# Kernel optimization log

Hardware: AMD Instinct MI355X
Metric: run time of the kernel (lower is better)

Reference implementation:

```python
import jax, jax.numpy as jnp
import numpy as np

B, T, D, E, V = 16, 256, 512, 512, 32000  # batch, seqlen, embed_dim, encoder_embed_dim, vocab


def setup_inputs() -> dict:
    key = jax.random.key(0)
    ks = jax.random.split(key, 13)
    s = 0.05
    return {
        "prev_output_tokens": jax.random.randint(ks[0], (B, T), 0, V),
        "encoder_out": jax.random.normal(ks[1], (B, E), jnp.float32),
        "embed": jax.random.normal(ks[2], (V, D), jnp.float32) * s,
        "W_ih0": jax.random.normal(ks[3], (4 * D, E + D), jnp.float32) * s,
        "W_hh0": jax.random.normal(ks[4], (4 * D, D), jnp.float32) * s,
        "b_ih0": jax.random.normal(ks[5], (4 * D,), jnp.float32) * s,
        "b_hh0": jax.random.normal(ks[6], (4 * D,), jnp.float32) * s,
        "W_ih1": jax.random.normal(ks[7], (4 * D, D), jnp.float32) * s,
        "W_hh1": jax.random.normal(ks[8], (4 * D, D), jnp.float32) * s,
        "b_ih1": jax.random.normal(ks[9], (4 * D,), jnp.float32) * s,
        "b_hh1": jax.random.normal(ks[10], (4 * D,), jnp.float32) * s,
        "W_out": jax.random.normal(ks[11], (V, D), jnp.float32) * s,
        "b_out": jax.random.normal(ks[12], (V,), jnp.float32) * s,
    }


def _lstm_cell(x, h, c, W_ih, W_hh, b_ih, b_hh):
    # torch.nn.LSTMCell gate order: i, f, g, o
    gates = x @ W_ih.T + b_ih + h @ W_hh.T + b_hh
    i, f, g, o = jnp.split(gates, 4, axis=-1)
    c_new = jax.nn.sigmoid(f) * c + jax.nn.sigmoid(i) * jnp.tanh(g)
    h_new = jax.nn.sigmoid(o) * jnp.tanh(c_new)
    return h_new, c_new


def reference(prev_output_tokens, encoder_out, embed, W_ih0, W_hh0, b_ih0, b_hh0,
              W_ih1, W_hh1, b_ih1, b_hh1, W_out, b_out):
    # padding_idx=0 -> row 0 of the embedding table is zero
    embed = embed.at[0].set(0.0)
    x = embed[prev_output_tokens]          # [B, T, D]  (dropout: eval mode -> identity)
    x = jnp.swapaxes(x, 0, 1)              # [T, B, D]
    bsz = x.shape[1]
    h0 = jnp.zeros((bsz, W_hh0.shape[1]), x.dtype)
    c0, h1, c1 = h0, h0, h0

    def step(carry, x_t):
        h0, c0, h1, c1 = carry
        inp = jnp.concatenate([x_t, encoder_out], axis=1)   # [B, D+E]
        h0, c0 = _lstm_cell(inp, h0, c0, W_ih0, W_hh0, b_ih0, b_hh0)
        h1, c1 = _lstm_cell(h0, h1, c1, W_ih1, W_hh1, b_ih1, b_hh1)
        return (h0, c0, h1, c1), h1

    _, outs = jax.lax.scan(step, (h0, c0, h1, c1), x)       # outs: [T, B, D]
    outs = jnp.swapaxes(outs, 0, 1)                          # [B, T, D]
    return outs @ W_out.T + b_out                            # [B, T, V]
```

## Files before the change

### kernel.cpp

```cpp
#include <hip/hip_runtime.h>
#include <hip/hip_bf16.h>
#include <math.h>

#define BB 16
#define TT 256
#define DD 512
#define EE 512
#define VV 32000
#define G4 2048
#define NTILES (16 * 2 * 250)

typedef __attribute__((ext_vector_type(4))) float f32x4;
typedef __attribute__((ext_vector_type(8))) short bf16x8;
typedef __attribute__((ext_vector_type(4))) unsigned u32x4;

union lf_u { u32x4 q; bf16x8 v; };

#define SENTMASK32 0x40004000u

__device__ __forceinline__ unsigned short f2bf(float x) {
    unsigned u = __float_as_uint(x);
    unsigned r = (u + 0x7FFFu + ((u >> 16) & 1u)) >> 16;
    return (unsigned short)r;
}

__device__ __forceinline__ float sigmoidf_(float x) { return 1.0f / (1.0f + expf(-x)); }

__global__ __launch_bounds__(256) void k_gather(const int* __restrict__ tok,
        const float* __restrict__ embed, unsigned short* __restrict__ Xb) {
    int m = blockIdx.x;
    int tk = tok[m];
    const float* src = embed + (size_t)tk * DD;
    int i = threadIdx.x * 2;
    float vx = 0.f, vy = 0.f;
    if (tk != 0) { float2 v = *(const float2*)&src[i]; vx = v.x; vy = v.y; }
    ushort2 o; o.x = f2bf(vx); o.y = f2bf(vy);
    *(ushort2*)&Xb[(size_t)m * DD + i] = o;
}

__global__ __launch_bounds__(256) void k_cvt(const float* __restrict__ in,
        unsigned short* __restrict__ out, int n4) {
    int i = blockIdx.x * 256 + threadIdx.x;
    if (i >= n4) return;
    float4 v = ((const float4*)in)[i];
    ushort4 o; o.x = f2bf(v.x); o.y = f2bf(v.y); o.z = f2bf(v.z); o.w = f2bf(v.w);
    ((ushort4*)out)[i] = o;
}

__global__ __launch_bounds__(256) void k_cvt_wih0x(const float* __restrict__ Wih0,
        unsigned short* __restrict__ out) {
    int i = blockIdx.x * 256 + threadIdx.x;
    int j = i >> 7;
    int k4 = (i & 127) << 2;
    float4 v = *(const float4*)&Wih0[(size_t)j * (EE + DD) + k4];
    ushort4 o; o.x = f2bf(v.x); o.y = f2bf(v.y); o.z = f2bf(v.z); o.w = f2bf(v.w);
    *(ushort4*)&out[(size_t)j * DD + k4] = o;
}

__global__ __launch_bounds__(256) void k_encterm(const float* __restrict__ enc,
        const float* __restrict__ Wih0, const float* __restrict__ bih0,
        const float* __restrict__ bhh0, float* __restrict__ et) {
    int b = blockIdx.x >> 3, jc = blockIdx.x & 7;
    int tid = threadIdx.x, lane = tid & 63, w = tid >> 6;
    __shared__ float es[EE];
    if (tid < EE / 4) *(float4*)&es[tid * 4] = *(const float4*)&enc[b * EE + tid * 4];
    __syncthreads();
    float4 e0 = *(const float4*)&es[lane * 4];
    float4 e1 = *(const float4*)&es[256 + lane * 4];
    for (int o = 0; o < 64; ++o) {
        int j = jc * 256 + w * 64 + o;
        const float4* Wr = (const float4*)&Wih0[(size_t)j * (EE + DD) + DD];
        float4 w0 = Wr[lane], w1 = Wr[64 + lane];
        float s = w0.x*e0.x + w0.y*e0.y + w0.z*e0.z + w0.w*e0.w
                + w1.x*e1.x + w1.y*e1.y + w1.z*e1.z + w1.w*e1.w;
        #pragma unroll
        for (int off = 32; off; off >>= 1) s += __shfl_xor(s, off);
        if (lane == 0) et[b * G4 + j] = s + bih0[j] + bhh0[j];
    }
}

__global__ __launch_bounds__(256) void k_gemm0(
        const unsigned short* __restrict__ A, const unsigned short* __restrict__ Bm,
        float* __restrict__ C, const float* __restrict__ extra,
        int M, int N, int K) {
    __shared__ __align__(16) unsigned short Alds[128 * 32];
    __shared__ __align__(16) unsigned short Blds[128 * 32];
    int tid = threadIdx.x, lane = tid & 63, w = tid >> 6;
    int wr = w >> 1, wc = w & 1;
    int nwgx = gridDim.x;
    int nwg = nwgx * gridDim.y;
    int lin = blockIdx.y * nwgx + blockIdx.x;
    int cpx = nwg >> 3;
    lin = (lin & 7) * cpx + (lin >> 3);
    int m0 = (lin % nwgx) * 128, n0 = (lin / nwgx) * 128;
    f32x4 acc[4][4];
    #pragma unroll
    for (int i = 0; i < 4; i++)
        #pragma unroll
        for (int j = 0; j < 4; j++) acc[i][j] = (f32x4)0.f;

    const char* Abase = (const char*)A;
    const char* Bbase = (const char*)Bm;
    for (int ks = 0; ks < K; ks += 32) {
        #pragma unroll
        for (int c = 0; c < 2; ++c) {
            int f = (tid + c * 256) * 16;
            int row = f >> 6;
            int inb = f & 63;
            const char* gA = Abase + (((size_t)(m0 + row) * K + ks) * 2 + inb);
            __builtin_amdgcn_global_load_lds(
                (const __attribute__((address_space(1))) void*)gA,
                (__attribute__((address_space(3))) void*)((char*)Alds + f), 16, 0, 0);
            const char* gB = Bbase + (((size_t)(n0 + row) * K + ks) * 2 + inb);
            __builtin_amdgcn_global_load_lds(
                (const __attribute__((address_space(1))) void*)gB,
                (__attribute__((address_space(3))) void*)((char*)Blds + f), 16, 0, 0);
        }
        __syncthreads();
        bf16x8 af[4], bfr[4];
        int r = lane & 15, ko = (lane >> 4) * 8;
        #pragma unroll
        for (int mi = 0; mi < 4; ++mi)
            af[mi] = *(const bf16x8*)&Alds[(wr * 64 + mi * 16 + r) * 32 + ko];
        #pragma unroll
        for (int ni = 0; ni < 4; ++ni)
            bfr[ni] = *(const bf16x8*)&Blds[(wc * 64 + ni * 16 + r) * 32 + ko];
        #pragma unroll
        for (int mi = 0; mi < 4; ++mi)
            #pragma unroll
            for (int ni = 0; ni < 4; ++ni)
                acc[mi][ni] = __builtin_amdgcn_mfma_f32_16x16x32_bf16(af[mi], bfr[ni], acc[mi][ni], 0, 0, 0);
        __syncthreads();
    }
    int cr = (lane >> 4) * 4, cc = lane & 15;
    #pragma unroll
    for (int mi = 0; mi < 4; ++mi) {
        #pragma unroll
        for (int ni = 0; ni < 4; ++ni) {
            int col = n0 + wc * 64 + ni * 16 + cc;
            #pragma unroll
            for (int rr = 0; rr < 4; ++rr) {
                int rowg = m0 + wr * 64 + mi * 16 + cr + rr;
                C[(size_t)rowg * N + col] = acc[mi][ni][rr] + extra[(rowg >> 8) * G4 + col];
            }
        }
    }
}

__device__ __forceinline__ void load16sc(const void* base, lf_u* o) {
    asm volatile(
        "global_load_dwordx4 %0, %16, off sc0 sc1\n\t"
        "global_load_dwordx4 %1, %16, off offset:64 sc0 sc1\n\t"
        "global_load_dwordx4 %2, %16, off offset:128 sc0 sc1\n\t"
        "global_load_dwordx4 %3, %16, off offset:192 sc0 sc1\n\t"
        "global_load_dwordx4 %4, %16, off offset:256 sc0 sc1\n\t"
        "global_load_dwordx4 %5, %16, off offset:320 sc0 sc1\n\t"
        "global_load_dwordx4 %6, %16, off offset:384 sc0 sc1\n\t"
        "global_load_dwordx4 %7, %16, off offset:448 sc0 sc1\n\t"
        "global_load_dwordx4 %8, %16, off offset:512 sc0 sc1\n\t"
        "global_load_dwordx4 %9, %16, off offset:576 sc0 sc1\n\t"
        "global_load_dwordx4 %10, %16, off offset:640 sc0 sc1\n\t"
        "global_load_dwordx4 %11, %16, off offset:704 sc0 sc1\n\t"
        "global_load_dwordx4 %12, %16, off offset:768 sc0 sc1\n\t"
        "global_load_dwordx4 %13, %16, off offset:832 sc0 sc1\n\t"
        "global_load_dwordx4 %14, %16, off offset:896 sc0 sc1\n\t"
        "global_load_dwordx4 %15, %16, off offset:960 sc0 sc1\n\t"
        "s_waitcnt vmcnt(0)"
        : "=&v"(o[0].q), "=&v"(o[1].q), "=&v"(o[2].q), "=&v"(o[3].q),
          "=&v"(o[4].q), "=&v"(o[5].q), "=&v"(o[6].q), "=&v"(o[7].q),
          "=&v"(o[8].q), "=&v"(o[9].q), "=&v"(o[10].q), "=&v"(o[11].q),
          "=&v"(o[12].q), "=&v"(o[13].q), "=&v"(o[14].q), "=&v"(o[15].q)
        : "v"(base)
        : "memory");
}

__device__ __forceinline__ void poll16sc(const void* base, lf_u* o) {
    for (;;) {
        load16sc(base, o);
        unsigned bad = 0;
        #pragma unroll
        for (int kt = 0; kt < 16; ++kt)
            bad |= (o[kt].q.x | o[kt].q.y | o[kt].q.z | o[kt].q.w);
        if (!__any((bad & SENTMASK32) != 0)) return;
    }
}

__device__ __forceinline__ void store8sc(void* addr, unsigned long long v) {
    asm volatile("global_store_dwordx2 %0, %1, off sc0 sc1"
                 :: "v"(addr), "v"(v) : "memory");
}

__global__ __launch_bounds__(256) void k_mega(
        const float* __restrict__ Gx,
        const float* __restrict__ Whh0,
        const float* __restrict__ Wih1, const float* __restrict__ Whh1,
        const float* __restrict__ bih1, const float* __restrict__ bhh1,
        unsigned short* h0hist, unsigned short* outsb,
        const unsigned short* zbuf,
        const unsigned short* __restrict__ Woutb, const float* __restrict__ bout,
        float* __restrict__ out,
        int* ep1, int* tick) {
    __shared__ __align__(16) unsigned char smem[4 * 32 * 512 * 2 + 512];
    __shared__ int idSh;
    const int bid = blockIdx.x;

    if (bid < 64) {
        unsigned short* wfrag = (unsigned short*)smem;
        unsigned short* houts = (unsigned short*)(smem + 4 * 32 * 512 * 2);
        const int l = threadIdx.x;
        const int role = bid >> 5;
        const int blk = bid & 31;
        const int d0 = blk * 16;
        const int r16 = l & 15;
        const int q = (l >> 4) & 3;
        const int ksub = q * 8;
        const int b0 = q * 4;
        const int srow = (l >> 2) & 15;
        const int sseg = l & 3;

        const int nkt = role ? 32 : 16;
        if (l < 64) {
            for (int tile = 0; tile < 4; ++tile) {
                int j = tile * 512 + d0 + r16;
                for (int kt = 0; kt < nkt; ++kt) {
                    const float* src;
                    if (role == 0)    src = Whh0 + (size_t)j * DD + kt * 32 + ksub;
                    else if (kt < 16) src = Wih1 + (size_t)j * DD + kt * 32 + ksub;
                    else              src = Whh1 + (size_t)j * DD + (kt - 16) * 32 + ksub;
                    float4 x = *(const float4*)src;
                    float4 y = *(const float4*)(src + 4);
                    bf16x8 w;
                    w[0] = f2bf(x.x); w[1] = f2bf(x.y); w[2] = f2bf(x.z); w[3] = f2bf(x.w);
                    w[4] = f2bf(y.x); w[5] = f2bf(y.y); w[6] = f2bf(y.z); w[7] = f2bf(y.w);
                    *(bf16x8*)&wfrag[((tile * 32 + kt) * 64 + l) * 8] = w;
                }
            }
        }
        __syncthreads();
        if (l >= 64) return;

        float cst[4] = {0.f, 0.f, 0.f, 0.f};
        lf_u xf[16];

        if (role == 0) {
            for (int t = 0; t < TT; ++t) {
                float gx[4][4];
                #pragma unroll
                for (int ni = 0; ni < 4; ++ni)
                    #pragma unroll
                    for (int rr = 0; rr < 4; ++rr)
                        gx[ni][rr] = Gx[((size_t)(b0 + rr) * TT + t) * G4 + ni * 512 + d0 + r16];

                const char* xb = (const char*)(h0hist + (size_t)t * (BB * DD) + r16 * DD) + q * 16;
                poll16sc(xb, xf);

                f32x4 acc[4];
                #pragma unroll
                for (int ni = 0; ni < 4; ++ni) acc[ni] = (f32x4)0.f;
                #pragma unroll
                for (int kt = 0; kt < 16; ++kt) {
                    #pragma unroll
                    for (int ni = 0; ni < 4; ++ni) {
                        bf16x8 wf = *(const bf16x8*)&wfrag[((ni * 32 + kt) * 64 + l) * 8];
                        acc[ni] = __builtin_amdgcn_mfma_f32_16x16x32_bf16(xf[kt].v, wf, acc[ni], 0, 0, 0);
                    }
                }
                #pragma unroll
                for (int rr = 0; rr < 4; ++rr) {
                    float gi = acc[0][rr] + gx[0][rr], gf = acc[1][rr] + gx[1][rr];
                    float gg = acc[2][rr] + gx[2][rr], go = acc[3][rr] + gx[3][rr];
                    float cn = sigmoidf_(gf) * cst[rr] + sigmoidf_(gi) * tanhf(gg);
                    float hn = sigmoidf_(go) * tanhf(cn);
                    cst[rr] = cn;
                    houts[(b0 + rr) * 16 + r16] = f2bf(hn);
                }
                asm volatile("" ::: "memory");
                {
                    const unsigned short* hp = &houts[srow * 16 + sseg * 4];
                    unsigned long long w8 =  (unsigned long long)hp[0]
                                          | ((unsigned long long)hp[1] << 16)
                                          | ((unsigned long long)hp[2] << 32)
                                          | ((unsigned long long)hp[3] << 48);
                    store8sc(h0hist + (size_t)(t + 1) * (BB * DD) + srow * DD + d0 + sseg * 4, w8);
                }
            }
        } else {
            lf_u hf[16];
            float bin[4];
            #pragma unroll
            for (int ni = 0; ni < 4; ++ni)
                bin[ni] = bih1[ni * 512 + d0 + r16] + bhh1[ni * 512 + d0 + r16];
            for (int t = 0; t < TT; ++t) {
                const char* xb = (const char*)(h0hist + (size_t)(t + 1) * (BB * DD) + r16 * DD) + q * 16;
                poll16sc(xb, xf);

                f32x4 acc[4];
                #pragma unroll
                for (int ni = 0; ni < 4; ++ni)
                    acc[ni] = (f32x4){bin[ni], bin[ni], bin[ni], bin[ni]};
                #pragma unroll
                for (int kt = 0; kt < 16; ++kt) {
                    #pragma unroll
                    for (int ni = 0; ni < 4; ++ni) {
                        bf16x8 wf = *(const bf16x8*)&wfrag[((ni * 32 + kt) * 64 + l) * 8];
                        acc[ni] = __builtin_amdgcn_mfma_f32_16x16x32_bf16(xf[kt].v, wf, acc[ni], 0, 0, 0);
                    }
                }
                const char* hb = (t == 0)
                    ? (const char*)(zbuf + r16 * DD) + q * 16
                    : (const char*)(outsb + ((size_t)r16 * TT + (t - 1)) * DD) + q * 16;
                poll16sc(hb, hf);
                #pragma unroll
                for (int kt = 0; kt < 16; ++kt) {
                    #pragma unroll
                    for (int ni = 0; ni < 4; ++ni) {
                        bf16x8 wf = *(const bf16x8*)&wfrag[((ni * 32 + 16 + kt) * 64 + l) * 8];
                        acc[ni] = __builtin_amdgcn_mfma_f32_16x16x32_bf16(hf[kt].v, wf, acc[ni], 0, 0, 0);
                    }
                }
                #pragma unroll
                for (int rr = 0; rr < 4; ++rr) {
                    float gi = acc[0][rr], gf = acc[1][rr], gg = acc[2][rr], go = acc[3][rr];
                    float cn = sigmoidf_(gf) * cst[rr] + sigmoidf_(gi) * tanhf(gg);
                    float hn = sigmoidf_(go) * tanhf(cn);
                    cst[rr] = cn;
                    houts[(b0 + rr) * 16 + r16] = f2bf(hn);
                }
                asm volatile("" ::: "memory");
                {
                    const unsigned short* hp = &houts[srow * 16 + sseg * 4];
                    unsigned long long w8 =  (unsigned long long)hp[0]
                                          | ((unsigned long long)hp[1] << 16)
                                          | ((unsigned long long)hp[2] << 32)
                                          | ((unsigned long long)hp[3] << 48);
                    store8sc(outsb + ((size_t)srow * TT + t) * DD + d0 + sseg * 4, w8);
                }
                asm volatile("s_waitcnt vmcnt(0)" ::: "memory");
                if (l == 0) {
                    int tv = t + 1;
                    asm volatile("global_store_dword %0, %1, off sc0 sc1"
                                 :: "v"(ep1 + blk * 16), "v"(tv) : "memory");
                }
            }
        }
    } else {
        unsigned short* Alds = (unsigned short*)smem;
        unsigned short* Blds = (unsigned short*)(smem + 8192);
        const int tid = threadIdx.x, lane = tid & 63, w = tid >> 6;
        const int wr = w >> 1, wc = w & 1;

        for (;;) {
            if (tid == 0) idSh = atomicAdd(tick, 1);
            __syncthreads();
            int id = idSh;
            if (id >= NTILES) break;

            int chunk = id / 500;
            int rem   = id % 500;
            int bg    = rem / 250;
            int nt    = rem % 250;
            int t0 = chunk * 16;
            int n0 = nt * 128;
            int target = t0 + 16;

            for (;;) {
                int v;
                asm volatile("global_load_dword %0, %1, off sc0 sc1\n\ts_waitcnt vmcnt(0)"
                             : "=v"(v) : "v"(ep1 + (lane & 31) * 16) : "memory");
                if (__all(v >= target)) break;
                __builtin_amdgcn_s_sleep(4);
            }

            f32x4 acc[4][4];
            #pragma unroll
            for (int i = 0; i < 4; i++)
                #pragma unroll
                for (int j = 0; j < 4; j++) acc[i][j] = (f32x4)0.f;

            for (int ks = 0; ks < DD; ks += 32) {
                #pragma unroll
                for (int c = 0; c < 2; ++c) {
                    int f = (tid + c * 256) * 16;
                    int row = f >> 6;
                    int inb = f & 63;
                    int bb = bg * 8 + (row >> 4);
                    int tt = t0 + (row & 15);
                    const char* gA = (const char*)outsb +
                        (((size_t)bb * TT + tt) * DD + ks) * 2 + inb;
                    __builtin_amdgcn_global_load_lds(
                        (const __attribute__((address_space(1))) void*)gA,
                        (__attribute__((address_space(3))) void*)((char*)Alds + f), 16, 0, 0);
                    const char* gB = (const char*)Woutb +
                        (((size_t)(n0 + row)) * DD + ks) * 2 + inb;
                    __builtin_amdgcn_global_load_lds(
                        (const __attribute__((address_space(1))) void*)gB,
                        (__attribute__((address_space(3))) void*)((char*)Blds + f), 16, 0, 0);
                }
                __syncthreads();
                bf16x8 af[4], bfr[4];
                int r = lane & 15, ko = (lane >> 4) * 8;
                #pragma unroll
                for (int mi = 0; mi < 4; ++mi)
                    af[mi] = *(const bf16x8*)&Alds[(wr * 64 + mi * 16 + r) * 32 + ko];
                #pragma unroll
                for (int ni = 0; ni < 4; ++ni)
                    bfr[ni] = *(const bf16x8*)&Blds[(wc * 64 + ni * 16 + r) * 32 + ko];
                #pragma unroll
                for (int mi = 0; mi < 4; ++mi)
                    #pragma unroll
                    for (int ni = 0; ni < 4; ++ni)
                        acc[mi][ni] = __builtin_amdgcn_mfma_f32_16x16x32_bf16(af[mi], bfr[ni], acc[mi][ni], 0, 0, 0);
                __syncthreads();
            }
            int cr = (lane >> 4) * 4, cc = lane & 15;
            #pragma unroll
            for (int mi = 0; mi < 4; ++mi) {
                #pragma unroll
                for (int ni = 0; ni < 4; ++ni) {
                    int col = n0 + wc * 64 + ni * 16 + cc;
                    #pragma unroll
                    for (int rr = 0; rr < 4; ++rr) {
                        int rloc = wr * 64 + mi * 16 + cr + rr;
                        int bb = bg * 8 + (rloc >> 4);
                        int tt = t0 + (rloc & 15);
                        out[((size_t)bb * TT + tt) * VV + col] = acc[mi][ni][rr] + bout[col];
                    }
                }
            }
        }
    }
}

extern "C" void kernel_launch(void* const* d_in, const int* in_sizes, int n_in,
                              void* d_out, int out_size, void* d_ws, size_t ws_size,
                              hipStream_t stream) {
    const int*   tok   = (const int*)  d_in[0];
    const float* enc   = (const float*)d_in[1];
    const float* embed = (const float*)d_in[2];
    const float* Wih0  = (const float*)d_in[3];
    const float* Whh0  = (const float*)d_in[4];
    const float* bih0  = (const float*)d_in[5];
    const float* bhh0  = (const float*)d_in[6];
    const float* Wih1  = (const float*)d_in[7];
    const float* Whh1  = (const float*)d_in[8];
    const float* bih1  = (const float*)d_in[9];
    const float* bhh1  = (const float*)d_in[10];
    const float* Wout  = (const float*)d_in[11];
    const float* bout  = (const float*)d_in[12];
    float* out = (float*)d_out;

    char* ws = (char*)d_ws;
    size_t off = 0;
    auto alloc = [&](size_t bytes) -> char* {
        char* p = ws + off; off += (bytes + 255) & ~(size_t)255; return p;
    };
    unsigned short* Xb     = (unsigned short*)alloc((size_t)BB * TT * DD * 2);
    unsigned short* Wih0xb = (unsigned short*)alloc((size_t)G4 * DD * 2);
    unsigned short* Woutb  = (unsigned short*)alloc((size_t)VV * DD * 2);
    float*          et     = (float*)alloc((size_t)BB * G4 * sizeof(float));
    float*          Gx     = (float*)alloc((size_t)BB * TT * G4 * sizeof(float));
    unsigned short* outsb  = (unsigned short*)alloc((size_t)BB * TT * DD * 2);
    unsigned short* h0hist = (unsigned short*)alloc((size_t)(TT + 1) * BB * DD * 2);
    unsigned short* zbuf   = (unsigned short*)alloc((size_t)BB * DD * 2);
    int*            ep1    = (int*)alloc(32 * 16 * sizeof(int));
    int*            tick   = (int*)alloc(64 * sizeof(int));

    hipMemsetAsync(h0hist, 0, (size_t)BB * DD * 2, stream);
    hipMemsetAsync(h0hist + (size_t)BB * DD, 0xFF, (size_t)TT * BB * DD * 2, stream);
    hipMemsetAsync(outsb, 0xFF, (size_t)BB * TT * DD * 2, stream);
    hipMemsetAsync(zbuf, 0, (size_t)BB * DD * 2, stream);
    hipMemsetAsync(ep1, 0, 32 * 16 * sizeof(int), stream);
    hipMemsetAsync(tick, 0, 64 * sizeof(int), stream);

    k_gather<<<BB * TT, 256, 0, stream>>>(tok, embed, Xb);
    k_cvt<<<(VV * DD / 4 + 255) / 256, 256, 0, stream>>>(Wout, Woutb, VV * DD / 4);
    k_cvt_wih0x<<<(G4 * DD / 4) / 256, 256, 0, stream>>>(Wih0, Wih0xb);
    k_encterm<<<BB * 8, 256, 0, stream>>>(enc, Wih0, bih0, bhh0, et);

    dim3 g1(BB * TT / 128, G4 / 128);
    k_gemm0<<<g1, 256, 0, stream>>>(Xb, Wih0xb, Gx, et, BB * TT, G4, DD);

    k_mega<<<256, 256, 0, stream>>>(Gx, Whh0, Wih1, Whh1, bih1, bhh1,
                                    h0hist, outsb, zbuf,
                                    Woutb, bout, out, ep1, tick);
}
```

Measured before the change: 1.592 ms.

## Fuse prep kernels and overlap W_out conversion and epoch signaling with recurrence

```diff
diff --git a/kernel.cpp b/kernel.cpp
--- a/kernel.cpp
+++ b/kernel.cpp
@@ -8,6 +8,7 @@
 #define EE 512
 #define VV 32000
 #define G4 2048
+#define NWORK 192
 #define NTILES (16 * 2 * 250)
 
 typedef __attribute__((ext_vector_type(4))) float f32x4;
@@ -17,6 +18,7 @@
 union lf_u { u32x4 q; bf16x8 v; };
 
 #define SENTMASK32 0x40004000u
+#define SENTMASK64 0x4000400040004000ULL
 
 __device__ __forceinline__ unsigned short f2bf(float x) {
     unsigned u = __float_as_uint(x);
@@ -26,56 +28,48 @@
 
 __device__ __forceinline__ float sigmoidf_(float x) { return 1.0f / (1.0f + expf(-x)); }
 
-__global__ __launch_bounds__(256) void k_gather(const int* __restrict__ tok,
-        const float* __restrict__ embed, unsigned short* __restrict__ Xb) {
-    int m = blockIdx.x;
-    int tk = tok[m];
-    const float* src = embed + (size_t)tk * DD;
-    int i = threadIdx.x * 2;
-    float vx = 0.f, vy = 0.f;
-    if (tk != 0) { float2 v = *(const float2*)&src[i]; vx = v.x; vy = v.y; }
-    ushort2 o; o.x = f2bf(vx); o.y = f2bf(vy);
-    *(ushort2*)&Xb[(size_t)m * DD + i] = o;
-}
-
-__global__ __launch_bounds__(256) void k_cvt(const float* __restrict__ in,
-        unsigned short* __restrict__ out, int n4) {
-    int i = blockIdx.x * 256 + threadIdx.x;
-    if (i >= n4) return;
-    float4 v = ((const float4*)in)[i];
-    ushort4 o; o.x = f2bf(v.x); o.y = f2bf(v.y); o.z = f2bf(v.z); o.w = f2bf(v.w);
-    ((ushort4*)out)[i] = o;
-}
-
-__global__ __launch_bounds__(256) void k_cvt_wih0x(const float* __restrict__ Wih0,
-        unsigned short* __restrict__ out) {
-    int i = blockIdx.x * 256 + threadIdx.x;
-    int j = i >> 7;
-    int k4 = (i & 127) << 2;
-    float4 v = *(const float4*)&Wih0[(size_t)j * (EE + DD) + k4];
-    ushort4 o; o.x = f2bf(v.x); o.y = f2bf(v.y); o.z = f2bf(v.z); o.w = f2bf(v.w);
-    *(ushort4*)&out[(size_t)j * DD + k4] = o;
-}
-
-__global__ __launch_bounds__(256) void k_encterm(const float* __restrict__ enc,
-        const float* __restrict__ Wih0, const float* __restrict__ bih0,
+__global__ __launch_bounds__(256) void k_prep(
+        const int* __restrict__ tok, const float* __restrict__ embed,
+        unsigned short* __restrict__ Xb,
+        const float* __restrict__ Wih0, unsigned short* __restrict__ Wih0xb,
+        const float* __restrict__ enc, const float* __restrict__ bih0,
         const float* __restrict__ bhh0, float* __restrict__ et) {
-    int b = blockIdx.x >> 3, jc = blockIdx.x & 7;
-    int tid = threadIdx.x, lane = tid & 63, w = tid >> 6;
     __shared__ float es[EE];
-    if (tid < EE / 4) *(float4*)&es[tid * 4] = *(const float4*)&enc[b * EE + tid * 4];
-    __syncthreads();
-    float4 e0 = *(const float4*)&es[lane * 4];
-    float4 e1 = *(const float4*)&es[256 + lane * 4];
-    for (int o = 0; o < 64; ++o) {
-        int j = jc * 256 + w * 64 + o;
-        const float4* Wr = (const float4*)&Wih0[(size_t)j * (EE + DD) + DD];
-        float4 w0 = Wr[lane], w1 = Wr[64 + lane];
-        float s = w0.x*e0.x + w0.y*e0.y + w0.z*e0.z + w0.w*e0.w
-                + w1.x*e1.x + w1.y*e1.y + w1.z*e1.z + w1.w*e1.w;
-        #pragma unroll
-        for (int off = 32; off; off >>= 1) s += __shfl_xor(s, off);
-        if (lane == 0) et[b * G4 + j] = s + bih0[j] + bhh0[j];
+    const int blk = blockIdx.x;
+    const int tid = threadIdx.x;
+    if (blk < BB * TT) {
+        int tk = tok[blk];
+        const float* src = embed + (size_t)tk * DD;
+        int i = tid * 2;
+        float vx = 0.f, vy = 0.f;
+        if (tk != 0) { float2 v = *(const float2*)&src[i]; vx = v.x; vy = v.y; }
+        ushort2 o; o.x = f2bf(vx); o.y = f2bf(vy);
+        *(ushort2*)&Xb[(size_t)blk * DD + i] = o;
+    } else if (blk < BB * TT + 1024) {
+        int i = (blk - BB * TT) * 256 + tid;
+        int j = i >> 7;
+        int k4 = (i & 127) << 2;
+        float4 v = *(const float4*)&Wih0[(size_t)j * (EE + DD) + k4];
+        ushort4 o; o.x = f2bf(v.x); o.y = f2bf(v.y); o.z = f2bf(v.z); o.w = f2bf(v.w);
+        *(ushort4*)&Wih0xb[(size_t)j * DD + k4] = o;
+    } else {
+        int bidx = blk - (BB * TT + 1024);
+        int b = bidx >> 3, jc = bidx & 7;
+        int lane = tid & 63, w = tid >> 6;
+        if (tid < EE / 4) *(float4*)&es[tid * 4] = *(const float4*)&enc[b * EE + tid * 4];
+        __syncthreads();
+        float4 e0 = *(const float4*)&es[lane * 4];
+        float4 e1 = *(const float4*)&es[256 + lane * 4];
+        for (int o = 0; o < 64; ++o) {
+            int j = jc * 256 + w * 64 + o;
+            const float4* Wr = (const float4*)&Wih0[(size_t)j * (EE + DD) + DD];
+            float4 w0 = Wr[lane], w1 = Wr[64 + lane];
+            float s = w0.x*e0.x + w0.y*e0.y + w0.z*e0.z + w0.w*e0.w
+                    + w1.x*e1.x + w1.y*e1.y + w1.z*e1.z + w1.w*e1.w;
+            #pragma unroll
+            for (int off = 32; off; off >>= 1) s += __shfl_xor(s, off);
+            if (lane == 0) et[b * G4 + j] = s + bih0[j] + bhh0[j];
+        }
     }
 }
 
@@ -197,9 +191,9 @@
         const float* __restrict__ bih1, const float* __restrict__ bhh1,
         unsigned short* h0hist, unsigned short* outsb,
         const unsigned short* zbuf,
-        const unsigned short* __restrict__ Woutb, const float* __restrict__ bout,
-        float* __restrict__ out,
-        int* ep1, int* tick) {
+        const float* __restrict__ Wout, unsigned short* Woutb,
+        const float* __restrict__ bout, float* __restrict__ out,
+        int* ep1, int* tick, int* wdone) {
     __shared__ __align__(16) unsigned char smem[4 * 32 * 512 * 2 + 512];
     __shared__ int idSh;
     const int bid = blockIdx.x;
@@ -237,7 +231,31 @@
             }
         }
         __syncthreads();
-        if (l >= 64) return;
+
+        if (l >= 64) {
+            if (role == 1 && l < 128) {
+                const int lw = l - 64;
+                const int ob = lw >> 2;
+                const int oseg = lw & 3;
+                const char* base = (const char*)(outsb + ((size_t)ob * TT) * DD + d0 + oseg * 4);
+                for (int t = 0; t < TT; ++t) {
+                    const void* addr = base + (size_t)t * DD * 2;
+                    for (;;) {
+                        unsigned long long v;
+                        asm volatile("global_load_dwordx2 %0, %1, off sc0 sc1\n\ts_waitcnt vmcnt(0)"
+                                     : "=v"(v) : "v"(addr) : "memory");
+                        if (!__any((v & SENTMASK64) != 0)) break;
+                        __builtin_amdgcn_s_sleep(2);
+                    }
+                    if (lw == 0) {
+                        int tv = t + 1;
+                        asm volatile("global_store_dword %0, %1, off sc0 sc1"
+                                     :: "v"(ep1 + blk * 16), "v"(tv) : "memory");
+                    }
+                }
+            }
+            return;
+        }
 
         float cst[4] = {0.f, 0.f, 0.f, 0.f};
         lf_u xf[16];
@@ -335,12 +353,6 @@
                                           | ((unsigned long long)hp[3] << 48);
                     store8sc(outsb + ((size_t)srow * TT + t) * DD + d0 + sseg * 4, w8);
                 }
-                asm volatile("s_waitcnt vmcnt(0)" ::: "memory");
-                if (l == 0) {
-                    int tv = t + 1;
-                    asm volatile("global_store_dword %0, %1, off sc0 sc1"
-                                 :: "v"(ep1 + blk * 16), "v"(tv) : "memory");
-                }
             }
         }
     } else {
@@ -348,6 +360,29 @@
         unsigned short* Blds = (unsigned short*)(smem + 8192);
         const int tid = threadIdx.x, lane = tid & 63, w = tid >> 6;
         const int wr = w >> 1, wc = w & 1;
+        const int wid = bid - 64;
+
+        for (size_t i = (size_t)wid * 256 + tid; i < (size_t)VV * DD / 4;
+             i += (size_t)NWORK * 256) {
+            float4 v = ((const float4*)Wout)[i];
+            unsigned long long pk =  (unsigned long long)f2bf(v.x)
+                                  | ((unsigned long long)f2bf(v.y) << 16)
+                                  | ((unsigned long long)f2bf(v.z) << 32)
+                                  | ((unsigned long long)f2bf(v.w) << 48);
+            store8sc(Woutb + i * 4, pk);
+        }
+        asm volatile("s_waitcnt vmcnt(0)" ::: "memory");
+        if (tid == 0) {
+            atomicAdd(wdone, 1);
+            for (;;) {
+                int v;
+                asm volatile("global_load_dword %0, %1, off sc0 sc1\n\ts_waitcnt vmcnt(0)"
+                             : "=v"(v) : "v"(wdone) : "memory");
+                if (v >= NWORK) break;
+                __builtin_amdgcn_s_sleep(8);
+            }
+        }
+        __syncthreads();
 
         for (;;) {
             if (tid == 0) idSh = atomicAdd(tick, 1);
@@ -368,7 +403,7 @@
                 asm volatile("global_load_dword %0, %1, off sc0 sc1\n\ts_waitcnt vmcnt(0)"
                              : "=v"(v) : "v"(ep1 + (lane & 31) * 16) : "memory");
                 if (__all(v >= target)) break;
-                __builtin_amdgcn_s_sleep(4);
+                __builtin_amdgcn_s_sleep(32);
             }
 
             f32x4 acc[4][4];
@@ -464,6 +499,7 @@
     unsigned short* zbuf   = (unsigned short*)alloc((size_t)BB * DD * 2);
     int*            ep1    = (int*)alloc(32 * 16 * sizeof(int));
     int*            tick   = (int*)alloc(64 * sizeof(int));
+    int*            wdone  = (int*)alloc(64 * sizeof(int));
 
     hipMemsetAsync(h0hist, 0, (size_t)BB * DD * 2, stream);
     hipMemsetAsync(h0hist + (size_t)BB * DD, 0xFF, (size_t)TT * BB * DD * 2, stream);
@@ -471,16 +507,15 @@
     hipMemsetAsync(zbuf, 0, (size_t)BB * DD * 2, stream);
     hipMemsetAsync(ep1, 0, 32 * 16 * sizeof(int), stream);
     hipMemsetAsync(tick, 0, 64 * sizeof(int), stream);
-
-    k_gather<<<BB * TT, 256, 0, stream>>>(tok, embed, Xb);
-    k_cvt<<<(VV * DD / 4 + 255) / 256, 256, 0, stream>>>(Wout, Woutb, VV * DD / 4);
-    k_cvt_wih0x<<<(G4 * DD / 4) / 256, 256, 0, stream>>>(Wih0, Wih0xb);
-    k_encterm<<<BB * 8, 256, 0, stream>>>(enc, Wih0, bih0, bhh0, et);
+    hipMemsetAsync(wdone, 0, 64 * sizeof(int), stream);
+
+    k_prep<<<BB * TT + 1024 + 128, 256, 0, stream>>>(
+        tok, embed, Xb, Wih0, Wih0xb, enc, bih0, bhh0, et);
 
     dim3 g1(BB * TT / 128, G4 / 128);
     k_gemm0<<<g1, 256, 0, stream>>>(Xb, Wih0xb, Gx, et, BB * TT, G4, DD);
 
     k_mega<<<256, 256, 0, stream>>>(Gx, Whh0, Wih1, Whh1, bih1, bhh1,
                                     h0hist, outsb, zbuf,
-                                    Woutb, bout, out, ep1, tick);
-}
+                                    Wout, Woutb, bout, out, ep1, tick, wdone);
+}
```

Result: faster. 1.522 ms, median of 2 (-4.4%).
